# Optimization experiments

Hardware: AMD Instinct MI355X
Metric: run time of the kernel (lower is better)

The kernel has to match this reference:

```python
import jax, jax.numpy as jnp
import numpy as np

HEAD_SIZE = 64
NUM_HEADS = 8
D_MODEL = NUM_HEADS * HEAD_SIZE  # 512
B, T = 8, 1024
LN_EPS = 1e-3  # tf.keras LayerNormalization default epsilon


def setup_inputs() -> dict:
    key = jax.random.key(0)
    ks = jax.random.split(key, 10)
    s = 0.02
    return {
        "inputs": jax.random.normal(ks[0], (B, T, D_MODEL), jnp.float32),
        "pos": jax.random.normal(ks[1], (B, T, D_MODEL), jnp.float32),
        "gamma": jnp.ones((D_MODEL,), jnp.float32),
        "beta": jnp.zeros((D_MODEL,), jnp.float32),
        "query_kernel": jax.random.normal(ks[2], (NUM_HEADS, D_MODEL, HEAD_SIZE), jnp.float32) * s,
        "key_kernel": jax.random.normal(ks[3], (NUM_HEADS, D_MODEL, HEAD_SIZE), jnp.float32) * s,
        "value_kernel": jax.random.normal(ks[4], (NUM_HEADS, D_MODEL, HEAD_SIZE), jnp.float32) * s,
        "pos_kernel": jax.random.normal(ks[5], (NUM_HEADS, D_MODEL, HEAD_SIZE), jnp.float32) * s,
        "pos_bias_u": jax.random.normal(ks[6], (NUM_HEADS, HEAD_SIZE), jnp.float32) * s,
        "pos_bias_v": jax.random.normal(ks[7], (NUM_HEADS, HEAD_SIZE), jnp.float32) * s,
        "projection_kernel": jax.random.normal(ks[8], (NUM_HEADS, HEAD_SIZE, D_MODEL), jnp.float32) * s,
        "projection_bias": jnp.zeros((D_MODEL,), jnp.float32),
    }


def _layer_norm(x, gamma, beta):
    mean = jnp.mean(x, axis=-1, keepdims=True)
    var = jnp.mean(jnp.square(x - mean), axis=-1, keepdims=True)
    return (x - mean) * jax.lax.rsqrt(var + LN_EPS) * gamma + beta


def _relative_shift(x):
    # Transformer-XL shift trick: x is [B, H, N, M]
    b, h, n, m = x.shape
    x = jnp.pad(x, ((0, 0), (0, 0), (0, 0), (1, 0)))  # [B,H,N,M+1]
    x = x.reshape(b, h, m + 1, n)
    return x[:, :, 1:, :].reshape(b, h, n, m)


def reference(inputs, pos, gamma, beta, query_kernel, key_kernel, value_kernel,
              pos_kernel, pos_bias_u, pos_bias_v, projection_kernel, projection_bias):
    x = _layer_norm(inputs, gamma, beta)
    # per-head projections: [B,N,I] x [H,I,O] -> [B,N,H,O]
    q = jnp.einsum("bni,hio->bnho", x, query_kernel)
    k = jnp.einsum("bni,hio->bnho", x, key_kernel)
    v = jnp.einsum("bni,hio->bnho", x, value_kernel)
    p = jnp.einsum("bmi,hio->bmho", pos, pos_kernel)
    # content and position scores (Transformer-XL / Conformer relmha)
    matrix_ac = jnp.einsum("bnho,bmho->bhnm", q + pos_bias_u, k)
    matrix_bd = _relative_shift(jnp.einsum("bnho,bmho->bhnm", q + pos_bias_v, p))
    scores = (matrix_ac + matrix_bd) / jnp.sqrt(jnp.asarray(HEAD_SIZE, x.dtype))
    attn = jax.nn.softmax(scores, axis=-1)
    out = jnp.einsum("bhnm,bmho->bnho", attn, v)
    out = jnp.einsum("bnho,hoi->bni", out, projection_kernel) + projection_bias
    # dropout_prob=0 / inference -> identity; residual add
    return inputs + out
```

## Files before the change

kernel.cpp:

```cpp
#include <hip/hip_runtime.h>

#define BB 8
#define TT 1024
#define DD 512
#define HH 8
#define HS 64

typedef __attribute__((ext_vector_type(8))) short short8;
typedef __attribute__((ext_vector_type(4))) float f32x4;
typedef __attribute__((ext_vector_type(16))) float f32x16;

#if __has_builtin(__builtin_amdgcn_exp2f)
#define EXP2(x) __builtin_amdgcn_exp2f(x)
#else
#define EXP2(x) exp2f(x)
#endif

__device__ __forceinline__ float bf2f(unsigned short u) {
  union { unsigned int i; float f; } v; v.i = ((unsigned int)u) << 16; return v.f;
}
__device__ __forceinline__ unsigned short f2bf(float f) {
  union { float f; unsigned int i; } v; v.f = f;
  unsigned int i = v.i;
  return (unsigned short)((i + 0x7FFFu + ((i >> 16) & 1u)) >> 16);
}
__device__ __forceinline__ unsigned int cvt_pk_bf16(float lo, float hi) {
  unsigned int r;
  asm volatile("v_cvt_pk_bf16_f32 %0, %1, %2" : "=v"(r) : "v"(lo), "v"(hi));
  return r;
}

__device__ __forceinline__ size_t x16(int r, int k) {
  return (size_t)(r >> 4) * 8192 + ((k >> 5) * 512) + (((k >> 3) & 3) * 128) + ((r & 15) * 8) + (k & 7);
}
__device__ __forceinline__ size_t t32_addr(int n, int k) {
  return (size_t)(n >> 5) * 2048 + ((k >> 4) * 512) + (((k >> 3) & 1) * 256) + ((n & 31) * 8) + (k & 7);
}
__device__ __forceinline__ size_t t16_addr(int n, int k) {
  return (size_t)(n >> 4) * 1024 + ((k >> 5) * 512) + (((k >> 3) & 3) * 128) + ((n & 15) * 8) + (k & 7);
}
__device__ __forceinline__ size_t vt_addr(int o, int m) {
  int s15 = (m & 3) | ((m & 4) << 1) | ((m & 8) >> 1);
  return (size_t)(m >> 5) * 2048 + (((m >> 4) & 1) * 1024) + ((o >> 5) * 512) +
         (((s15 >> 3) & 1) * 256) + ((o & 31) * 8) + (s15 & 7);
}

__global__ __launch_bounds__(256) void prep(const float* __restrict__ in,
                                            const float* __restrict__ pos,
                                            const float* __restrict__ gamma,
                                            const float* __restrict__ beta,
                                            const float* __restrict__ Wq, const float* __restrict__ Wk,
                                            const float* __restrict__ Wv, const float* __restrict__ Wp,
                                            const float* __restrict__ Wo,
                                            unsigned short* __restrict__ x,
                                            unsigned short* __restrict__ p16,
                                            unsigned short* __restrict__ Tq, unsigned short* __restrict__ Tk,
                                            unsigned short* __restrict__ Tv, unsigned short* __restrict__ Tp,
                                            unsigned short* __restrict__ Two) {
  int t = threadIdx.x;
  if (blockIdx.y == 2) {
    int g = blockIdx.x;
    if (g >= 40) return;
    int sel = g >> 3, gg = g & 7;
    if (sel < 4) {
      const float* win = sel == 0 ? Wq : sel == 1 ? Wk : sel == 2 ? Wv : Wp;
      unsigned short* wout = sel == 0 ? Tq : sel == 1 ? Tk : sel == 2 ? Tv : Tp;
      for (int idx = t; idx < 32768; idx += 256) {
        int of = idx >> 13, kk = (idx >> 9) & 15, l4 = (idx >> 7) & 3, l15 = (idx >> 3) & 15, e = idx & 7;
        int o = of * 16 + l15, k = kk * 32 + l4 * 8 + e;
        wout[(size_t)gg * 32768 + idx] = f2bf(win[(size_t)gg * 32768 + k * 64 + o]);
      }
    } else {
      for (int idx = t; idx < 32768; idx += 256) {
        int of = idx >> 13, kk = (idx >> 9) & 15, l4 = (idx >> 7) & 3, l15 = (idx >> 3) & 15, e = idx & 7;
        int i = gg * 64 + of * 16 + l15, k = kk * 32 + l4 * 8 + e;
        Two[(size_t)gg * 32768 + idx] = f2bf(Wo[(size_t)k * 512 + i]);
      }
    }
    return;
  }
  int rt = blockIdx.x;
  int ri = t >> 4, ki = t & 15;
  if (blockIdx.y == 0) {
    const float* rp = in + ((size_t)rt * 16 + ri) * DD + ki * 32;
    float v[32];
#pragma unroll
    for (int j = 0; j < 8; ++j) *(float4*)&v[j * 4] = *(const float4*)(rp + j * 4);
    float s = 0.f;
#pragma unroll
    for (int j = 0; j < 32; ++j) s += v[j];
    s += __shfl_xor(s, 1); s += __shfl_xor(s, 2); s += __shfl_xor(s, 4); s += __shfl_xor(s, 8);
    float mean = s * (1.0f / DD);
    float vs = 0.f;
#pragma unroll
    for (int j = 0; j < 32; ++j) { float d = v[j] - mean; vs += d * d; }
    vs += __shfl_xor(vs, 1); vs += __shfl_xor(vs, 2); vs += __shfl_xor(vs, 4); vs += __shfl_xor(vs, 8);
    float inv = rsqrtf(vs * (1.0f / DD) + 1e-3f);
    size_t base = (size_t)rt * 8192 + ki * 512 + ri * 8;
#pragma unroll
    for (int qg = 0; qg < 4; ++qg) {
      short8 u;
#pragma unroll
      for (int e = 0; e < 8; ++e) {
        int col = ki * 32 + qg * 8 + e;
        u[e] = (short)f2bf((v[qg * 8 + e] - mean) * inv * gamma[col] + beta[col]);
      }
      *(short8*)(x + base + qg * 128) = u;
    }
  } else {
    const float* rp = pos + ((size_t)rt * 16 + ri) * DD + ki * 32;
    size_t base = (size_t)rt * 8192 + ki * 512 + ri * 8;
#pragma unroll
    for (int qg = 0; qg < 4; ++qg) {
      float4 a = *(const float4*)(rp + qg * 8);
      float4 b = *(const float4*)(rp + qg * 8 + 4);
      short8 u;
      u[0] = (short)f2bf(a.x); u[1] = (short)f2bf(a.y); u[2] = (short)f2bf(a.z); u[3] = (short)f2bf(a.w);
      u[4] = (short)f2bf(b.x); u[5] = (short)f2bf(b.y); u[6] = (short)f2bf(b.z); u[7] = (short)f2bf(b.w);
      *(short8*)(p16 + base + qg * 128) = u;
    }
  }
}

#define MF16(a, b, c) __builtin_amdgcn_mfma_f32_16x16x32_bf16(a, b, c, 0, 0, 0)

__global__ __launch_bounds__(512) void proj2(const unsigned short* __restrict__ X,
                                             const unsigned short* __restrict__ POS,
                                             const unsigned short* __restrict__ Wtq,
                                             const unsigned short* __restrict__ Wtk,
                                             const unsigned short* __restrict__ Wtv,
                                             const unsigned short* __restrict__ Wtp,
                                             const float* __restrict__ bu,
                                             const float* __restrict__ bv,
                                             unsigned short* __restrict__ QU,
                                             unsigned short* __restrict__ QV,
                                             unsigned short* __restrict__ KT,
                                             unsigned short* __restrict__ VT,
                                             unsigned short* __restrict__ PT) {
  __shared__ __align__(16) unsigned short Wlds[32768];
  int tid = threadIdx.x;
  int w = tid >> 6, l = tid & 63;
  int l15 = l & 15, l4 = l >> 4;
  int rb = blockIdx.x, h = blockIdx.y, sel = blockIdx.z;
  const unsigned short* Wsrc = (sel == 0 ? Wtq : sel == 1 ? Wtk : sel == 2 ? Wtv : Wtp) + (size_t)h * 32768;
  const unsigned short* A = (sel == 3) ? POS : X;
#pragma unroll
  for (int i = 0; i < 8; ++i)
    *(short8*)(Wlds + (tid + i * 512) * 8) = *(const short8*)(Wsrc + (tid + i * 512) * 8);
  __syncthreads();

  int rt0 = rb * 32 + w * 4;
  f32x4 acc[4][4];
#pragma unroll
  for (int j4 = 0; j4 < 4; ++j4)
#pragma unroll
    for (int of = 0; of < 4; ++of) acc[j4][of] = (f32x4){0.f, 0.f, 0.f, 0.f};
  for (int kk = 0; kk < 16; ++kk) {
    short8 a0 = *(const short8*)(A + (size_t)(rt0 + 0) * 8192 + kk * 512 + l * 8);
    short8 a1 = *(const short8*)(A + (size_t)(rt0 + 1) * 8192 + kk * 512 + l * 8);
    short8 a2 = *(const short8*)(A + (size_t)(rt0 + 2) * 8192 + kk * 512 + l * 8);
    short8 a3 = *(const short8*)(A + (size_t)(rt0 + 3) * 8192 + kk * 512 + l * 8);
    const unsigned short* wp = Wlds + kk * 512 + l * 8;
    short8 w0 = *(const short8*)(wp);
    short8 w1 = *(const short8*)(wp + 8192);
    short8 w2 = *(const short8*)(wp + 16384);
    short8 w3 = *(const short8*)(wp + 24576);
    acc[0][0] = MF16(a0, w0, acc[0][0]); acc[0][1] = MF16(a0, w1, acc[0][1]);
    acc[0][2] = MF16(a0, w2, acc[0][2]); acc[0][3] = MF16(a0, w3, acc[0][3]);
    acc[1][0] = MF16(a1, w0, acc[1][0]); acc[1][1] = MF16(a1, w1, acc[1][1]);
    acc[1][2] = MF16(a1, w2, acc[1][2]); acc[1][3] = MF16(a1, w3, acc[1][3]);
    acc[2][0] = MF16(a2, w0, acc[2][0]); acc[2][1] = MF16(a2, w1, acc[2][1]);
    acc[2][2] = MF16(a2, w2, acc[2][2]); acc[2][3] = MF16(a2, w3, acc[2][3]);
    acc[3][0] = MF16(a3, w0, acc[3][0]); acc[3][1] = MF16(a3, w1, acc[3][1]);
    acc[3][2] = MF16(a3, w2, acc[3][2]); acc[3][3] = MF16(a3, w3, acc[3][3]);
  }

  if (sel == 0) {
    const float S = 0.125f * 1.44269504088896f;
#pragma unroll
    for (int of = 0; of < 4; ++of) {
      int o = of * 16 + l15;
      float bum = bu[h * HS + o], bvm = bv[h * HS + o];
#pragma unroll
      for (int j4 = 0; j4 < 4; ++j4)
#pragma unroll
        for (int j = 0; j < 4; ++j) {
          int r = (rt0 + j4) * 16 + l4 * 4 + j;
          int b = r >> 10, n = r & 1023;
          size_t bho = ((size_t)b * HH + h) * 65536;
          QU[bho + t32_addr(n, o)] = f2bf((acc[j4][of][j] + bum) * S);
          QV[bho + t16_addr(n, o)] = f2bf((acc[j4][of][j] + bvm) * S);
        }
    }
  } else if (sel == 1) {
#pragma unroll
    for (int of = 0; of < 4; ++of) {
      int o = of * 16 + l15;
#pragma unroll
      for (int j4 = 0; j4 < 4; ++j4)
#pragma unroll
        for (int j = 0; j < 4; ++j) {
          int r = (rt0 + j4) * 16 + l4 * 4 + j;
          int b = r >> 10, n = r & 1023;
          KT[((size_t)b * HH + h) * 65536 + t32_addr(n, o)] = f2bf(acc[j4][of][j]);
        }
    }
  } else if (sel == 2) {
#pragma unroll
    for (int of = 0; of < 4; ++of) {
      int o = of * 16 + l15;
#pragma unroll
      for (int j4 = 0; j4 < 4; ++j4)
#pragma unroll
        for (int j = 0; j < 4; ++j) {
          int r = (rt0 + j4) * 16 + l4 * 4 + j;
          int b = r >> 10, m = r & 1023;
          VT[((size_t)b * HH + h) * 65536 + vt_addr(o, m)] = f2bf(acc[j4][of][j]);
        }
    }
  } else {
#pragma unroll
    for (int of = 0; of < 4; ++of) {
      int o = of * 16 + l15;
#pragma unroll
      for (int j4 = 0; j4 < 4; ++j4)
#pragma unroll
        for (int j = 0; j < 4; ++j) {
          int r = (rt0 + j4) * 16 + l4 * 4 + j;
          int b = r >> 10, n = r & 1023;
          PT[((size_t)b * HH + h) * 65536 + t16_addr(n, o)] = f2bf(acc[j4][of][j]);
        }
    }
  }
}

__global__ __launch_bounds__(512) void out2(const unsigned short* __restrict__ A,
                                            const unsigned short* __restrict__ WoTT,
                                            const float* __restrict__ resid,
                                            const float* __restrict__ bias,
                                            float* __restrict__ Out) {
  __shared__ __align__(16) unsigned short Wlds[32768];
  int tid = threadIdx.x;
  int w = tid >> 6, l = tid & 63;
  int l15 = l & 15, l4 = l >> 4;
  int rb = blockIdx.x, cb = blockIdx.y;
  const unsigned short* Wsrc = WoTT + (size_t)cb * 32768;
#pragma unroll
  for (int i = 0; i < 8; ++i)
    *(short8*)(Wlds + (tid + i * 512) * 8) = *(const short8*)(Wsrc + (tid + i * 512) * 8);
  __syncthreads();

  int rt0 = rb * 32 + w * 4;
  f32x4 acc[4][4];
#pragma unroll
  for (int j4 = 0; j4 < 4; ++j4)
#pragma unroll
    for (int of = 0; of < 4; ++of) acc[j4][of] = (f32x4){0.f, 0.f, 0.f, 0.f};
  for (int kk = 0; kk < 16; ++kk) {
    short8 a0 = *(const short8*)(A + (size_t)(rt0 + 0) * 8192 + kk * 512 + l * 8);
    short8 a1 = *(const short8*)(A + (size_t)(rt0 + 1) * 8192 + kk * 512 + l * 8);
    short8 a2 = *(const short8*)(A + (size_t)(rt0 + 2) * 8192 + kk * 512 + l * 8);
    short8 a3 = *(const short8*)(A + (size_t)(rt0 + 3) * 8192 + kk * 512 + l * 8);
    const unsigned short* wp = Wlds + kk * 512 + l * 8;
    short8 w0 = *(const short8*)(wp);
    short8 w1 = *(const short8*)(wp + 8192);
    short8 w2 = *(const short8*)(wp + 16384);
    short8 w3 = *(const short8*)(wp + 24576);
    acc[0][0] = MF16(a0, w0, acc[0][0]); acc[0][1] = MF16(a0, w1, acc[0][1]);
    acc[0][2] = MF16(a0, w2, acc[0][2]); acc[0][3] = MF16(a0, w3, acc[0][3]);
    acc[1][0] = MF16(a1, w0, acc[1][0]); acc[1][1] = MF16(a1, w1, acc[1][1]);
    acc[1][2] = MF16(a1, w2, acc[1][2]); acc[1][3] = MF16(a1, w3, acc[1][3]);
    acc[2][0] = MF16(a2, w0, acc[2][0]); acc[2][1] = MF16(a2, w1, acc[2][1]);
    acc[2][2] = MF16(a2, w2, acc[2][2]); acc[2][3] = MF16(a2, w3, acc[2][3]);
    acc[3][0] = MF16(a3, w0, acc[3][0]); acc[3][1] = MF16(a3, w1, acc[3][1]);
    acc[3][2] = MF16(a3, w2, acc[3][2]); acc[3][3] = MF16(a3, w3, acc[3][3]);
  }
#pragma unroll
  for (int of = 0; of < 4; ++of) {
    int i = cb * 64 + of * 16 + l15;
    float bi = bias[i];
#pragma unroll
    for (int j4 = 0; j4 < 4; ++j4)
#pragma unroll
      for (int j = 0; j < 4; ++j) {
        int r = (rt0 + j4) * 16 + l4 * 4 + j;
        Out[(size_t)r * DD + i] = acc[j4][of][j] + bi + resid[(size_t)r * DD + i];
      }
  }
}

#define WLS 1036
__global__ __launch_bounds__(512, 4) void attn_mfma(const unsigned short* __restrict__ QT,
                                                    const unsigned short* __restrict__ QVT,
                                                    const unsigned short* __restrict__ KT,
                                                    const unsigned short* __restrict__ VT,
                                                    const unsigned short* __restrict__ PT,
                                                    unsigned short* __restrict__ pre) {
  int i = blockIdx.x;
  int slot = i >> 3;
  int p = (i & 7) * 8 + (slot >> 5);
  int nb = slot & 31;
  int b = p >> 3, h = p & 7;
  int n0 = nb * 32;
  __shared__ __align__(16) unsigned short Wl[34][WLS];
  int tid = threadIdx.x;
  int w = tid >> 6, l = tid & 63;
  int l15 = l & 15, l4 = l >> 4;
  int l31 = l & 31, hi = l >> 5;
  size_t bh = ((size_t)b * HH + h) * 65536;
  const unsigned short* QTb = QT  + bh;
  const unsigned short* QVb = QVT + bh;
  const unsigned short* KTb = KT  + bh;
  const unsigned short* PTb = PT  + bh;
  const unsigned short* VTb = VT  + bh;

  if (tid < 32) {
    int m = n0 + tid + 1;
    if (m <= TT - 1) Wl[tid][m] = 0;
  }
  {
    int rg = w >> 2, ch = w & 3;
    const unsigned short* abase = QVb + (size_t)(nb * 2 + rg) * 1024 + l * 8;
    short8 a0 = *(const short8*)(abase);
    short8 a1 = *(const short8*)(abase + 512);
    for (int cg = 0; cg < 16; ++cg) {
      int ct = ch * 16 + cg;
      const unsigned short* bbase = PTb + (size_t)ct * 1024 + l * 8;
      f32x4 acc = {0.f, 0.f, 0.f, 0.f};
      acc = MF16(a0, *(const short8*)(bbase), acc);
      acc = MF16(a1, *(const short8*)(bbase + 512), acc);
      int c = ct * 16 + l15;
#pragma unroll
      for (int j = 0; j < 4; ++j) {
        int rr = 16 * rg + l4 * 4 + j;
        unsigned short v = f2bf(acc[j]);
        int m1 = c + n0 + rr - (TT - 1);
        if (m1 >= 0) Wl[rr][m1] = v;
        int m2 = c + n0 + rr + 1;
        if (rr >= 1 && m2 <= TT - 1) Wl[rr - 1][m2] = v;
      }
    }
  }
  {
    int qr = n0 + 32 + l15; if (qr > TT - 1) qr = TT - 1;
    const unsigned short* abase = QVb + (size_t)(qr >> 4) * 1024 + l4 * 128 + (qr & 15) * 8;
    short8 a0 = *(const short8*)(abase);
    short8 a1 = *(const short8*)(abase + 512);
    for (int cg = 0; cg < 8; ++cg) {
      int ct = w * 8 + cg;
      const unsigned short* bbase = PTb + (size_t)ct * 1024 + l * 8;
      f32x4 acc = {0.f, 0.f, 0.f, 0.f};
      acc = MF16(a0, *(const short8*)(bbase), acc);
      acc = MF16(a1, *(const short8*)(bbase + 512), acc);
      if (l4 == 0) {
        int m2 = ct * 16 + l15 + n0 + 33;
        if (m2 <= TT - 1) Wl[31][m2] = f2bf(acc[0]);
      }
    }
  }
  __syncthreads();

  const unsigned short* qtb = QTb + (size_t)nb * 2048 + l * 8;
  short8 qb0 = *(const short8*)(qtb);
  short8 qb1 = *(const short8*)(qtb + 512);
  short8 qb2 = *(const short8*)(qtb + 1024);
  short8 qb3 = *(const short8*)(qtb + 1536);
  f32x16 Oa0 = {}, Oa1 = {};
  float run_l = 0.f;

  short8 kc0, kc1, kc2, kc3;
  {
    const unsigned short* ktb = KTb + (size_t)w * 2048 + l * 8;
    kc0 = *(const short8*)(ktb);
    kc1 = *(const short8*)(ktb + 512);
    kc2 = *(const short8*)(ktb + 1024);
    kc3 = *(const short8*)(ktb + 1536);
  }

#pragma unroll 1
  for (int ci = 0; ci < 4; ++ci) {
    int mt = ci * 8 + w;
    int m0 = mt * 32;
    const unsigned short* vtb = VTb + (size_t)mt * 2048 + l * 8;
    short8 vv0 = *(const short8*)(vtb);
    short8 vv1 = *(const short8*)(vtb + 1024);
    short8 vv2 = *(const short8*)(vtb + 512);
    short8 vv3 = *(const short8*)(vtb + 1536);
    f32x16 s;
#pragma unroll
    for (int g = 0; g < 4; ++g) {
      ushort4 bd4 = *(const ushort4*)&Wl[l31][m0 + 8 * g + 4 * hi];
      s[4 * g + 0] = bf2f(bd4.x);
      s[4 * g + 1] = bf2f(bd4.y);
      s[4 * g + 2] = bf2f(bd4.z);
      s[4 * g + 3] = bf2f(bd4.w);
    }
    s = __builtin_amdgcn_mfma_f32_32x32x16_bf16(kc0, qb0, s, 0, 0, 0);
    s = __builtin_amdgcn_mfma_f32_32x32x16_bf16(kc1, qb1, s, 0, 0, 0);
    s = __builtin_amdgcn_mfma_f32_32x32x16_bf16(kc2, qb2, s, 0, 0, 0);
    s = __builtin_amdgcn_mfma_f32_32x32x16_bf16(kc3, qb3, s, 0, 0, 0);
    if (ci < 3) {
      const unsigned short* kn = KTb + (size_t)(mt + 8) * 2048 + l * 8;
      kc0 = *(const short8*)(kn);
      kc1 = *(const short8*)(kn + 512);
      kc2 = *(const short8*)(kn + 1024);
      kc3 = *(const short8*)(kn + 1536);
    }
    float sum = 0.f;
#pragma unroll
    for (int i2 = 0; i2 < 16; ++i2) { s[i2] = EXP2(s[i2]); sum += s[i2]; }
    sum += __shfl_xor(sum, 32);
    run_l += sum;
    short8 bp0, bp1;
    {
      unsigned int* u = (unsigned int*)&bp0;
      u[0] = cvt_pk_bf16(s[0], s[1]);
      u[1] = cvt_pk_bf16(s[2], s[3]);
      u[2] = cvt_pk_bf16(s[4], s[5]);
      u[3] = cvt_pk_bf16(s[6], s[7]);
      unsigned int* v2 = (unsigned int*)&bp1;
      v2[0] = cvt_pk_bf16(s[8], s[9]);
      v2[1] = cvt_pk_bf16(s[10], s[11]);
      v2[2] = cvt_pk_bf16(s[12], s[13]);
      v2[3] = cvt_pk_bf16(s[14], s[15]);
    }
    Oa0 = __builtin_amdgcn_mfma_f32_32x32x16_bf16(vv0, bp0, Oa0, 0, 0, 0);
    Oa0 = __builtin_amdgcn_mfma_f32_32x32x16_bf16(vv1, bp1, Oa0, 0, 0, 0);
    Oa1 = __builtin_amdgcn_mfma_f32_32x32x16_bf16(vv2, bp0, Oa1, 0, 0, 0);
    Oa1 = __builtin_amdgcn_mfma_f32_32x32x16_bf16(vv3, bp1, Oa1, 0, 0, 0);
  }

  __syncthreads();
  float* WLf = (float*)&Wl[0][0];
  float* myO = WLf + w * 2176;
#pragma unroll
  for (int i2 = 0; i2 < 16; ++i2) {
    int o0 = (i2 & 3) + 8 * (i2 >> 2) + 4 * hi;
    myO[o0 * 33 + l31]        = Oa0[i2];
    myO[(o0 + 32) * 33 + l31] = Oa1[i2];
  }
  if (l < 32) myO[2112 + l] = run_l;
  __syncthreads();
#pragma unroll
  for (int q4 = 0; q4 < 4; ++q4) {
    int q = w * 4 + q4;
    float denom = 0.f, val = 0.f;
#pragma unroll
    for (int w2 = 0; w2 < 8; ++w2) {
      denom += WLf[w2 * 2176 + 2112 + q];
      val   += WLf[w2 * 2176 + l * 33 + q];
    }
    pre[x16(b * TT + n0 + q, h * HS + l)] = f2bf(val / denom);
  }
}

extern "C" void kernel_launch(void* const* d_in, const int* in_sizes, int n_in,
                              void* d_out, int out_size, void* d_ws, size_t ws_size,
                              hipStream_t stream) {
  const float* inputs = (const float*)d_in[0];
  const float* pos    = (const float*)d_in[1];
  const float* gamma  = (const float*)d_in[2];
  const float* beta   = (const float*)d_in[3];
  const float* Wq = (const float*)d_in[4];
  const float* Wk = (const float*)d_in[5];
  const float* Wv = (const float*)d_in[6];
  const float* Wp = (const float*)d_in[7];
  const float* bu = (const float*)d_in[8];
  const float* bv = (const float*)d_in[9];
  const float* Wo = (const float*)d_in[10];
  const float* bo = (const float*)d_in[11];
  float* out = (float*)d_out;
  unsigned short* w16 = (unsigned short*)d_ws;

  const size_t T2 = (size_t)BB * TT * DD;
  unsigned short* x_bf  = w16;
  unsigned short* pre_b = x_bf  + T2;
  unsigned short* QUp   = pre_b + T2;
  unsigned short* QVp   = QUp   + T2;
  unsigned short* Kp    = QVp   + T2;
  unsigned short* Vtp   = Kp    + T2;
  unsigned short* Pp    = Vtp   + T2;
  unsigned short* Pos16 = Pp    + T2;
  unsigned short* WtQ   = Pos16 + T2;
  unsigned short* WtK   = WtQ + 262144;
  unsigned short* WtV   = WtK + 262144;
  unsigned short* WtP   = WtV + 262144;
  unsigned short* WoTT  = WtP + 262144;

  prep<<<dim3(512, 3), dim3(256), 0, stream>>>(inputs, pos, gamma, beta, Wq, Wk, Wv, Wp, Wo,
                                               x_bf, Pos16, WtQ, WtK, WtV, WtP, WoTT);
  proj2<<<dim3(16, 8, 4), dim3(512), 0, stream>>>(x_bf, Pos16, WtQ, WtK, WtV, WtP, bu, bv,
                                                  QUp, QVp, Kp, Vtp, Pp);
  attn_mfma<<<dim3(2048), dim3(512), 0, stream>>>(QUp, QVp, Kp, Vtp, Pp, pre_b);
  out2<<<dim3(16, 8), dim3(512), 0, stream>>>(pre_b, WoTT, inputs, bo, out);
}
```

Before: 162.2 us.

## Compute positional score band with 32x32 MFMA and shared t32 layout

Switches the positional (QV·P) score computation in the attention kernel from 16x16x32 MFMA tiles to 32x32x16 tiles, storing QV and P in the same t32 layout used by QU/K so one address serves both. The extra row computation for the shift boundary is skipped when the block is at the end and its column loop is bounded to only the needed tiles. The aim is fewer MFMA issues and fewer operand loads per score, at the cost of a different scatter pattern into shared memory.

```diff
diff --git a/kernel.cpp b/kernel.cpp
--- a/kernel.cpp
+++ b/kernel.cpp
@@ -35,9 +35,6 @@
 }
 __device__ __forceinline__ size_t t32_addr(int n, int k) {
   return (size_t)(n >> 5) * 2048 + ((k >> 4) * 512) + (((k >> 3) & 1) * 256) + ((n & 31) * 8) + (k & 7);
-}
-__device__ __forceinline__ size_t t16_addr(int n, int k) {
-  return (size_t)(n >> 4) * 1024 + ((k >> 5) * 512) + (((k >> 3) & 3) * 128) + ((n & 15) * 8) + (k & 7);
 }
 __device__ __forceinline__ size_t vt_addr(int o, int m) {
   int s15 = (m & 3) | ((m & 4) << 1) | ((m & 8) >> 1);
@@ -123,6 +120,7 @@
 }
 
 #define MF16(a, b, c) __builtin_amdgcn_mfma_f32_16x16x32_bf16(a, b, c, 0, 0, 0)
+#define MF32(a, b, c) __builtin_amdgcn_mfma_f32_32x32x16_bf16(a, b, c, 0, 0, 0)
 
 __global__ __launch_bounds__(512) void proj2(const unsigned short* __restrict__ X,
                                              const unsigned short* __restrict__ POS,
@@ -188,8 +186,9 @@
           int r = (rt0 + j4) * 16 + l4 * 4 + j;
           int b = r >> 10, n = r & 1023;
           size_t bho = ((size_t)b * HH + h) * 65536;
-          QU[bho + t32_addr(n, o)] = f2bf((acc[j4][of][j] + bum) * S);
-          QV[bho + t16_addr(n, o)] = f2bf((acc[j4][of][j] + bvm) * S);
+          size_t ta = t32_addr(n, o);
+          QU[bho + ta] = f2bf((acc[j4][of][j] + bum) * S);
+          QV[bho + ta] = f2bf((acc[j4][of][j] + bvm) * S);
         }
     }
   } else if (sel == 1) {
@@ -228,7 +227,7 @@
         for (int j = 0; j < 4; ++j) {
           int r = (rt0 + j4) * 16 + l4 * 4 + j;
           int b = r >> 10, n = r & 1023;
-          PT[((size_t)b * HH + h) * 65536 + t16_addr(n, o)] = f2bf(acc[j4][of][j]);
+          PT[((size_t)b * HH + h) * 65536 + t32_addr(n, o)] = f2bf(acc[j4][of][j]);
         }
     }
   }
@@ -305,7 +304,6 @@
   __shared__ __align__(16) unsigned short Wl[34][WLS];
   int tid = threadIdx.x;
   int w = tid >> 6, l = tid & 63;
-  int l15 = l & 15, l4 = l >> 4;
   int l31 = l & 31, hi = l >> 5;
   size_t bh = ((size_t)b * HH + h) * 65536;
   const unsigned short* QTb = QT  + bh;
@@ -319,21 +317,25 @@
     if (m <= TT - 1) Wl[tid][m] = 0;
   }
   {
-    int rg = w >> 2, ch = w & 3;
-    const unsigned short* abase = QVb + (size_t)(nb * 2 + rg) * 1024 + l * 8;
-    short8 a0 = *(const short8*)(abase);
-    short8 a1 = *(const short8*)(abase + 512);
-    for (int cg = 0; cg < 16; ++cg) {
-      int ct = ch * 16 + cg;
-      const unsigned short* bbase = PTb + (size_t)ct * 1024 + l * 8;
-      f32x4 acc = {0.f, 0.f, 0.f, 0.f};
-      acc = MF16(a0, *(const short8*)(bbase), acc);
-      acc = MF16(a1, *(const short8*)(bbase + 512), acc);
-      int c = ct * 16 + l15;
-#pragma unroll
-      for (int j = 0; j < 4; ++j) {
-        int rr = 16 * rg + l4 * 4 + j;
-        unsigned short v = f2bf(acc[j]);
+    const unsigned short* aq = QVb + (size_t)nb * 2048 + l * 8;
+    short8 a0 = *(const short8*)(aq);
+    short8 a1 = *(const short8*)(aq + 512);
+    short8 a2 = *(const short8*)(aq + 1024);
+    short8 a3 = *(const short8*)(aq + 1536);
+#pragma unroll
+    for (int cg = 0; cg < 4; ++cg) {
+      int ct = w + 8 * cg;
+      const unsigned short* bp = PTb + (size_t)ct * 2048 + l * 8;
+      f32x16 acc = {};
+      acc = MF32(a0, *(const short8*)(bp),        acc);
+      acc = MF32(a1, *(const short8*)(bp + 512),  acc);
+      acc = MF32(a2, *(const short8*)(bp + 1024), acc);
+      acc = MF32(a3, *(const short8*)(bp + 1536), acc);
+      int c = ct * 32 + l31;
+#pragma unroll
+      for (int i2 = 0; i2 < 16; ++i2) {
+        int rr = (i2 & 3) + 8 * (i2 >> 2) + 4 * hi;
+        unsigned short v = f2bf(acc[i2]);
         int m1 = c + n0 + rr - (TT - 1);
         if (m1 >= 0) Wl[rr][m1] = v;
         int m2 = c + n0 + rr + 1;
@@ -341,19 +343,21 @@
       }
     }
   }
-  {
-    int qr = n0 + 32 + l15; if (qr > TT - 1) qr = TT - 1;
-    const unsigned short* abase = QVb + (size_t)(qr >> 4) * 1024 + l4 * 128 + (qr & 15) * 8;
-    short8 a0 = *(const short8*)(abase);
-    short8 a1 = *(const short8*)(abase + 512);
-    for (int cg = 0; cg < 8; ++cg) {
-      int ct = w * 8 + cg;
-      const unsigned short* bbase = PTb + (size_t)ct * 1024 + l * 8;
-      f32x4 acc = {0.f, 0.f, 0.f, 0.f};
-      acc = MF16(a0, *(const short8*)(bbase), acc);
-      acc = MF16(a1, *(const short8*)(bbase + 512), acc);
-      if (l4 == 0) {
-        int m2 = ct * 16 + l15 + n0 + 33;
+  if (n0 + 32 < TT) {
+    const unsigned short* aq = QVb + (size_t)(nb + 1) * 2048 + l * 8;
+    short8 a0 = *(const short8*)(aq);
+    short8 a1 = *(const short8*)(aq + 512);
+    short8 a2 = *(const short8*)(aq + 1024);
+    short8 a3 = *(const short8*)(aq + 1536);
+    for (int ct = w; ct * 32 <= 990 - n0; ct += 8) {
+      const unsigned short* bp = PTb + (size_t)ct * 2048 + l * 8;
+      f32x16 acc = {};
+      acc = MF32(a0, *(const short8*)(bp),        acc);
+      acc = MF32(a1, *(const short8*)(bp + 512),  acc);
+      acc = MF32(a2, *(const short8*)(bp + 1024), acc);
+      acc = MF32(a3, *(const short8*)(bp + 1536), acc);
+      if (hi == 0) {
+        int m2 = ct * 32 + l31 + n0 + 33;
         if (m2 <= TT - 1) Wl[31][m2] = f2bf(acc[0]);
       }
     }
@@ -395,10 +399,10 @@
       s[4 * g + 2] = bf2f(bd4.z);
       s[4 * g + 3] = bf2f(bd4.w);
     }
-    s = __builtin_amdgcn_mfma_f32_32x32x16_bf16(kc0, qb0, s, 0, 0, 0);
-    s = __builtin_amdgcn_mfma_f32_32x32x16_bf16(kc1, qb1, s, 0, 0, 0);
-    s = __builtin_amdgcn_mfma_f32_32x32x16_bf16(kc2, qb2, s, 0, 0, 0);
-    s = __builtin_amdgcn_mfma_f32_32x32x16_bf16(kc3, qb3, s, 0, 0, 0);
+    s = MF32(kc0, qb0, s);
+    s = MF32(kc1, qb1, s);
+    s = MF32(kc2, qb2, s);
+    s = MF32(kc3, qb3, s);
     if (ci < 3) {
       const unsigned short* kn = KTb + (size_t)(mt + 8) * 2048 + l * 8;
       kc0 = *(const short8*)(kn);
@@ -424,10 +428,10 @@
       v2[2] = cvt_pk_bf16(s[12], s[13]);
       v2[3] = cvt_pk_bf16(s[14], s[15]);
     }
-    Oa0 = __builtin_amdgcn_mfma_f32_32x32x16_bf16(vv0, bp0, Oa0, 0, 0, 0);
-    Oa0 = __builtin_amdgcn_mfma_f32_32x32x16_bf16(vv1, bp1, Oa0, 0, 0, 0);
-    Oa1 = __builtin_amdgcn_mfma_f32_32x32x16_bf16(vv2, bp0, Oa1, 0, 0, 0);
-    Oa1 = __builtin_amdgcn_mfma_f32_32x32x16_bf16(vv3, bp1, Oa1, 0, 0, 0);
+    Oa0 = MF32(vv0, bp0, Oa0);
+    Oa0 = MF32(vv1, bp1, Oa0);
+    Oa1 = MF32(vv2, bp0, Oa1);
+    Oa1 = MF32(vv3, bp1, Oa1);
   }
 
   __syncthreads();
```

New measurement: 153.0 us. 5.7% less time.
